# Kernel tuning notes

Hardware: AMD Instinct MI355X
Metric: run time of the kernel (lower is better)

## Reference

```python
import jax, jax.numpy as jnp
import numpy as np

EPS = 1e-5
D, C, T, H = 512, 256, 2, 2  # d_model, d_ctx, tokens, heads
HD = D // H                   # head dim


def _ln(x, g, b):
    m = x.mean(-1, keepdims=True)
    v = ((x - m) ** 2).mean(-1, keepdims=True)
    return (x - m) / jnp.sqrt(v + EPS) * g + b


def setup_inputs() -> dict:
    key = jax.random.key(0)
    ks = jax.random.split(key, 16)
    B, L = 8, 4096
    w = lambda k, s: (jax.random.normal(k, s, jnp.float32) * 0.02)
    Hc, H2 = 512, 1024  # ctx-head hidden = max(D,C); mix hidden = 2*D
    return {
        "x": jax.random.normal(ks[0], (B, L, D), jnp.float32),
        "context": jax.random.normal(ks[1], (B, C), jnp.float32),
        "pad_valid_mask": jax.random.bernoulli(ks[2], 0.9, (B, L)),
        "film_ln_g": jnp.ones(D), "film_ln_b": jnp.zeros(D),
        "film_w": w(ks[3], (2 * D, C)), "film_b": jnp.zeros(2 * D),
        "concat_w": w(ks[4], (D, D + C)), "concat_b": jnp.zeros(D),
        "concat_ln_g": jnp.ones(D), "concat_ln_b": jnp.zeros(D),
        "ctx_w1": w(ks[5], (Hc, C)), "ctx_b1": jnp.zeros(Hc),
        "ctx_w2": w(ks[6], (T * D, Hc)), "ctx_b2": jnp.zeros(T * D),
        "q_ln_g": jnp.ones(D), "q_ln_b": jnp.zeros(D),
        "in_proj_w": w(ks[7], (3 * D, D)), "in_proj_b": jnp.zeros(3 * D),
        "out_proj_w": w(ks[8], (D, D)), "out_proj_b": jnp.zeros(D),
        "mix_w1": w(ks[9], (H2, 4 * D)), "mix_b1": jnp.zeros(H2),
        "mix_w2": w(ks[10], (D, H2)), "mix_b2": jnp.zeros(D),
        "out_ln_g": jnp.ones(D), "out_ln_b": jnp.zeros(D),
        "gate_w": w(ks[11], (D, C)), "gate_b": jnp.zeros(D),
    }


def reference(x, context, pad_valid_mask,
              film_ln_g, film_ln_b, film_w, film_b,
              concat_w, concat_b, concat_ln_g, concat_ln_b,
              ctx_w1, ctx_b1, ctx_w2, ctx_b2,
              q_ln_g, q_ln_b, in_proj_w, in_proj_b, out_proj_w, out_proj_b,
              mix_w1, mix_b1, mix_w2, mix_b2,
              out_ln_g, out_ln_b, gate_w, gate_b):
    B, L, _ = x.shape
    film_gain, alpha_max = 1.0, 1.0
    # 1) HyperFiLM: base = (1 + gain*gamma) * LN(x) + gain*beta
    gb = context @ film_w.T + film_b                      # [B, 2D]
    gamma, beta = gb[:, :D], gb[:, D:]
    base = (1.0 + film_gain * gamma)[:, None, :] * _ln(x, film_ln_g, film_ln_b) \
           + (film_gain * beta)[:, None, :]
    # 2) Concat path
    ctx_exp = jnp.broadcast_to(context[:, None, :], (B, L, C))
    z = jnp.concatenate([x, ctx_exp], axis=-1)            # [B, L, D+C]
    upd_c = _ln(jax.nn.relu(z @ concat_w.T + concat_b), concat_ln_g, concat_ln_b)
    # 3) Cross-attn path: context -> T tokens
    h = jax.nn.gelu(context @ ctx_w1.T + ctx_b1, approximate=False)
    ctx_tok = (h @ ctx_w2.T + ctx_b2).reshape(B, T, D)
    x_q = _ln(x, q_ln_g, q_ln_b)
    wq, wk, wv = in_proj_w[:D], in_proj_w[D:2 * D], in_proj_w[2 * D:]
    bq, bk, bv = in_proj_b[:D], in_proj_b[D:2 * D], in_proj_b[2 * D:]
    q = (x_q @ wq.T + bq).reshape(B, L, H, HD)
    k = (ctx_tok @ wk.T + bk).reshape(B, T, H, HD)
    v = (ctx_tok @ wv.T + bv).reshape(B, T, H, HD)
    scores = jnp.einsum('blhd,bthd->bhlt', q, k) / jnp.sqrt(jnp.float32(HD))
    attn = jax.nn.softmax(scores, axis=-1)
    a = jnp.einsum('bhlt,bthd->blhd', attn, v).reshape(B, L, D)
    attn_out = a @ out_proj_w.T + out_proj_b
    mix_in = jnp.concatenate([x, attn_out, x - attn_out, x * attn_out], axis=-1)
    upd_a = jax.nn.relu(mix_in @ mix_w1.T + mix_b1) @ mix_w2.T + mix_b2
    # 4) Combine with sigmoid gate, alpha, pad mask
    gate = jax.nn.sigmoid(context @ gate_w.T + gate_b) * alpha_max  # [B, D]
    gate = gate[:, None, :] * pad_valid_mask[:, :, None].astype(x.dtype)
    out = _ln(base + gate * (upd_c + upd_a), out_ln_g, out_ln_b)
    return out
```

## Files before the change

kernel.cpp:

```cpp
#include <hip/hip_runtime.h>
#include <hip/hip_bf16.h>


#define N_TOK 32768
#define HALF_ROWS 16384

typedef unsigned short u16;
typedef __attribute__((ext_vector_type(8))) __bf16 bf16x8;
typedef __attribute__((ext_vector_type(4))) float f32x4;

__device__ __forceinline__ float bf2f(unsigned int h) { return __uint_as_float(h << 16); }
__device__ __forceinline__ u16 f2bf(float f) {
    unsigned int u = __float_as_uint(f);
    u += 0x7FFFu + ((u >> 16) & 1u);
    return (u16)(u >> 16);
}
__device__ __forceinline__ void load8(const u16* p, float* v) {
    uint4 u = *(const uint4*)p;
    v[0] = bf2f(u.x & 0xffffu); v[1] = bf2f(u.x >> 16);
    v[2] = bf2f(u.y & 0xffffu); v[3] = bf2f(u.y >> 16);
    v[4] = bf2f(u.z & 0xffffu); v[5] = bf2f(u.z >> 16);
    v[6] = bf2f(u.w & 0xffffu); v[7] = bf2f(u.w >> 16);
}
__device__ __forceinline__ uint4 pack8(const float* v) {
    uint4 u;
    u.x = (unsigned)f2bf(v[0]) | ((unsigned)f2bf(v[1]) << 16);
    u.y = (unsigned)f2bf(v[2]) | ((unsigned)f2bf(v[3]) << 16);
    u.z = (unsigned)f2bf(v[4]) | ((unsigned)f2bf(v[5]) << 16);
    u.w = (unsigned)f2bf(v[6]) | ((unsigned)f2bf(v[7]) << 16);
    return u;
}
__device__ __forceinline__ void async16(const u16* g, u16* lds) {
    __builtin_amdgcn_global_load_lds(
        (const __attribute__((address_space(1))) unsigned int*)g,
        (__attribute__((address_space(3))) unsigned int*)lds, 16, 0, 0);
}

__global__ void prep_kernel(const float* __restrict__ in_proj_w,
                            const float* __restrict__ in_proj_b,
                            const float* __restrict__ qb,
                            const float* __restrict__ concat_w,
                            const float* __restrict__ mix_w1,
                            const float* __restrict__ mix_w2,
                            const float* __restrict__ context,
                            float* __restrict__ bqp,
                            u16* __restrict__ cwbf, u16* __restrict__ m1bf,
                            u16* __restrict__ m2bf, u16* __restrict__ ctxbf) {
    const int bid = blockIdx.x;
    const int tid = threadIdx.x;
    if (bid < 128) {
        const int wave = tid >> 6, lane = tid & 63;
        const int j = bid * 4 + wave;
        const int i = lane * 8;
        float4 w0 = *(const float4*)(in_proj_w + (size_t)j * 512 + i);
        float4 w1 = *(const float4*)(in_proj_w + (size_t)j * 512 + i + 4);
        float4 b0 = *(const float4*)(qb + i);
        float4 b1 = *(const float4*)(qb + i + 4);
        float p1 = w0.x*b0.x + w0.y*b0.y + w0.z*b0.z + w0.w*b0.w
                 + w1.x*b1.x + w1.y*b1.y + w1.z*b1.z + w1.w*b1.w;
        for (int m = 1; m < 64; m <<= 1) p1 += __shfl_xor(p1, m, 64);
        if (lane == 0) bqp[j] = in_proj_b[j] + p1;
    } else if (bid < 320) {
        int i = (bid - 128) * 256 + tid;
        const float* s = concat_w + (size_t)i * 8;
        float4 a = *(const float4*)s;
        float4 b = *(const float4*)(s + 4);
        float v[8] = {a.x, a.y, a.z, a.w, b.x, b.y, b.z, b.w};
        *(uint4*)(cwbf + (size_t)i * 8) = pack8(v);
    } else if (bid < 576) {
        int i = (bid - 320) * 256 + tid;
        const float* s = mix_w2 + (size_t)i * 8;
        float4 a = *(const float4*)s;
        float4 b = *(const float4*)(s + 4);
        float v[8] = {a.x, a.y, a.z, a.w, b.x, b.y, b.z, b.w};
        *(uint4*)(m2bf + (size_t)i * 8) = pack8(v);
    } else if (bid < 1344) {
        int idx = (bid - 576) * 256 + tid;
        int n = idx / 192;
        int k = (idx - n * 192) * 8;
        const float* base = mix_w1 + (size_t)n * 2048;
        float v[8];
        if (k < 512) {
            #pragma unroll
            for (int e = 0; e < 8; e++) v[e] = base[k + e] + base[1024 + k + e];
        } else if (k < 1024) {
            #pragma unroll
            for (int e = 0; e < 8; e++) v[e] = base[k + e] - base[512 + k + e];
        } else {
            #pragma unroll
            for (int e = 0; e < 8; e++) v[e] = base[512 + k + e];
        }
        *(uint4*)(m1bf + (size_t)n * 1536 + k) = pack8(v);
    } else {
        for (int i = tid; i < 2048; i += 256)
            ctxbf[i] = f2bf(context[i]);
    }
}

__global__ void ctx_stage_a(const float* __restrict__ context,
                            const float* __restrict__ film_w, const float* __restrict__ film_b,
                            const float* __restrict__ gate_w, const float* __restrict__ gate_b,
                            const float* __restrict__ ctx_w1, const float* __restrict__ ctx_b1,
                            float* __restrict__ gb1, float* __restrict__ betab,
                            float* __restrict__ gateb, float* __restrict__ hbuf) {
    const int wave = threadIdx.x >> 6, lane = threadIdx.x & 63;
    const int widx = blockIdx.x * 4 + wave;
    const int b   = widx >> 11;
    const int j2  = widx & 2047;
    const int cat = j2 >> 9;
    const int j   = j2 & 511;
    const float* wrow;
    if      (cat == 0) wrow = film_w + (size_t)j * 256;
    else if (cat == 1) wrow = film_w + (size_t)(512 + j) * 256;
    else if (cat == 2) wrow = gate_w + (size_t)j * 256;
    else               wrow = ctx_w1 + (size_t)j * 256;
    float4 wv = *(const float4*)(wrow + lane * 4);
    float4 cv = *(const float4*)(context + b * 256 + lane * 4);
    float s = wv.x * cv.x + wv.y * cv.y + wv.z * cv.z + wv.w * cv.w;
    for (int m = 1; m < 64; m <<= 1) s += __shfl_xor(s, m, 64);
    if (lane == 0) {
        if      (cat == 0) gb1[b * 512 + j]   = 1.0f + s + film_b[j];
        else if (cat == 1) betab[b * 512 + j] = s + film_b[512 + j];
        else if (cat == 2) gateb[b * 512 + j] = 1.f / (1.f + expf(-(s + gate_b[j])));
        else {
            float hv = s + ctx_b1[j];
            hbuf[b * 512 + j] = 0.5f * hv * (1.0f + erff(hv * 0.70710678118654752f));
        }
    }
}

__global__ void ctx_stage_b(const float* __restrict__ hbuf,
                            const float* __restrict__ ctx_w2, const float* __restrict__ ctx_b2,
                            float* __restrict__ tokbuf) {
    const int wave = threadIdx.x >> 6, lane = threadIdx.x & 63;
    const int widx = blockIdx.x * 4 + wave;
    const int b = widx >> 10;
    const int j = widx & 1023;
    const float* wrow = ctx_w2 + (size_t)j * 512 + lane * 8;
    const float* hr   = hbuf + b * 512 + lane * 8;
    float4 w0 = *(const float4*)wrow, w1 = *(const float4*)(wrow + 4);
    float4 h0 = *(const float4*)hr,   h1 = *(const float4*)(hr + 4);
    float s = w0.x*h0.x + w0.y*h0.y + w0.z*h0.z + w0.w*h0.w
            + w1.x*h1.x + w1.y*h1.y + w1.z*h1.z + w1.w*h1.w;
    for (int m = 1; m < 64; m <<= 1) s += __shfl_xor(s, m, 64);
    if (lane == 0) tokbuf[b * 1024 + j] = s + ctx_b2[j];
}

__global__ void ctx_stage_c(const float* __restrict__ tokbuf,
                            const float* __restrict__ in_proj_w, const float* __restrict__ in_proj_b,
                            float* __restrict__ kbuf, float* __restrict__ vbuf) {
    const int wave = threadIdx.x >> 6, lane = threadIdx.x & 63;
    const int widx = blockIdx.x * 4 + wave;
    const int b  = widx >> 11;
    const int r  = widx & 2047;
    const int t  = r >> 10;
    const int kv = (r >> 9) & 1;
    const int j  = r & 511;
    const float* wrow = in_proj_w + (size_t)(512 + kv * 512 + j) * 512 + lane * 8;
    const float* tk   = tokbuf + (b * 2 + t) * 512 + lane * 8;
    float4 w0 = *(const float4*)wrow, w1 = *(const float4*)(wrow + 4);
    float4 t0 = *(const float4*)tk,   t1 = *(const float4*)(tk + 4);
    float s = w0.x*t0.x + w0.y*t0.y + w0.z*t0.z + w0.w*t0.w
            + w1.x*t1.x + w1.y*t1.y + w1.z*t1.z + w1.w*t1.w;
    for (int m = 1; m < 64; m <<= 1) s += __shfl_xor(s, m, 64);
    if (lane == 0) {
        float v = s + in_proj_b[512 + kv * 512 + j];
        if (kv == 0) kbuf[(b * 2 + t) * 512 + j] = v;
        else         vbuf[(b * 2 + t) * 512 + j] = v;
    }
}

__global__ void ctx_stage_d(const float* __restrict__ in_proj_w,
                            const float* __restrict__ out_proj_w,
                            const float* __restrict__ qg, const float* __restrict__ bqp,
                            const float* __restrict__ kbuf, const float* __restrict__ vbuf,
                            float* __restrict__ ubuf, float* __restrict__ vobuf,
                            float* __restrict__ subuf, float* __restrict__ c0buf) {
    const int tid = threadIdx.x;
    __shared__ float sh[256];
    __shared__ float red[256];
    if (blockIdx.x < 32) {
        const int bid = blockIdx.x;
        const int b = bid >> 2, idx = bid & 3;
        const int t = idx >> 1, h = idx & 1;
        sh[tid] = kbuf[(b * 2 + t) * 512 + h * 256 + tid];
        __syncthreads();
        float a0 = 0.f, a1 = 0.f;
        #pragma unroll 4
        for (int dd = 0; dd < 256; dd++) {
            const float kv = sh[dd];
            const float* wr = in_proj_w + (size_t)(h * 256 + dd) * 512;
            a0 += kv * wr[tid];
            a1 += kv * wr[tid + 256];
        }
        float u0 = a0 * qg[tid], u1 = a1 * qg[tid + 256];
        ubuf[bid * 512 + tid]       = u0;
        ubuf[bid * 512 + tid + 256] = u1;
        red[tid] = u0 + u1;
        __syncthreads();
        for (int s = 128; s > 0; s >>= 1) { if (tid < s) red[tid] += red[tid + s]; __syncthreads(); }
        if (tid == 0) subuf[bid] = red[0];
        __syncthreads();
        red[tid] = bqp[h * 256 + tid] * sh[tid];
        __syncthreads();
        for (int s = 128; s > 0; s >>= 1) { if (tid < s) red[tid] += red[tid + s]; __syncthreads(); }
        if (tid == 0) c0buf[bid] = red[0];
    } else {
        const int bid = blockIdx.x - 32;
        const int b = bid >> 2, idx = bid & 3;
        const int t = idx >> 1, h = idx & 1;
        sh[tid] = vbuf[(b * 2 + t) * 512 + h * 256 + tid];
        __syncthreads();
        const float* w0 = out_proj_w + (size_t)tid * 512 + h * 256;
        const float* w1 = out_proj_w + (size_t)(tid + 256) * 512 + h * 256;
        float acc0 = 0.f, acc1 = 0.f;
        #pragma unroll 2
        for (int dd = 0; dd < 256; dd += 4) {
            float4 x0 = *(const float4*)(w0 + dd);
            float4 x1 = *(const float4*)(w1 + dd);
            acc0 += x0.x*sh[dd] + x0.y*sh[dd+1] + x0.z*sh[dd+2] + x0.w*sh[dd+3];
            acc1 += x1.x*sh[dd] + x1.y*sh[dd+1] + x1.z*sh[dd+2] + x1.w*sh[dd+3];
        }
        vobuf[bid * 512 + tid]       = acc0;
        vobuf[bid * 512 + tid + 256] = acc1;
    }
}

__global__ void statsattn_kernel(const float* __restrict__ x, float* __restrict__ stats,
                                 u16* __restrict__ mixA, u16* __restrict__ pbufH,
                                 const float* __restrict__ ubuf, const float* __restrict__ subuf,
                                 const float* __restrict__ c0buf, const float* __restrict__ vobuf,
                                 const float* __restrict__ ob, const int rowbase) {
    const int wave = threadIdx.x >> 6, lane = threadIdx.x & 63;
    const size_t lr = (size_t)blockIdx.x * 8 + wave * 2;
    const size_t gr = lr + rowbase;
    const int b = (int)(gr >> 12);
    float v[2][8], s[2] = {0.f, 0.f}, ss[2] = {0.f, 0.f};
    #pragma unroll
    for (int r = 0; r < 2; r++) {
        const float* xr = x + (gr + r) * 512 + lane * 8;
        float4 a = *(const float4*)xr;
        float4 c = *(const float4*)(xr + 4);
        v[r][0]=a.x; v[r][1]=a.y; v[r][2]=a.z; v[r][3]=a.w;
        v[r][4]=c.x; v[r][5]=c.y; v[r][6]=c.z; v[r][7]=c.w;
        #pragma unroll
        for (int e = 0; e < 8; e++) { s[r] += v[r][e]; ss[r] += v[r][e] * v[r][e]; }
    }
    float u[4][8];
    #pragma unroll
    for (int idx = 0; idx < 4; idx++) {
        const float* up = ubuf + (b * 4 + idx) * 512 + lane * 8;
        float4 u0 = *(const float4*)up, u1 = *(const float4*)(up + 4);
        u[idx][0]=u0.x; u[idx][1]=u0.y; u[idx][2]=u0.z; u[idx][3]=u0.w;
        u[idx][4]=u1.x; u[idx][5]=u1.y; u[idx][6]=u1.z; u[idx][7]=u1.w;
    }
    float sd[2][4];
    #pragma unroll
    for (int r = 0; r < 2; r++)
        #pragma unroll
        for (int idx = 0; idx < 4; idx++) {
            float acc = 0.f;
            #pragma unroll
            for (int e = 0; e < 8; e++) acc += v[r][e] * u[idx][e];
            sd[r][idx] = acc;
        }
    for (int m = 1; m < 64; m <<= 1) {
        #pragma unroll
        for (int r = 0; r < 2; r++) {
            s[r] += __shfl_xor(s[r], m, 64); ss[r] += __shfl_xor(ss[r], m, 64);
            #pragma unroll
            for (int idx = 0; idx < 4; idx++) sd[r][idx] += __shfl_xor(sd[r][idx], m, 64);
        }
    }
    float vo[4][8];
    #pragma unroll
    for (int idx = 0; idx < 4; idx++) {
        const float* vp = vobuf + (b * 4 + idx) * 512 + lane * 8;
        float4 v0 = *(const float4*)vp, v1 = *(const float4*)(vp + 4);
        vo[idx][0]=v0.x; vo[idx][1]=v0.y; vo[idx][2]=v0.z; vo[idx][3]=v0.w;
        vo[idx][4]=v1.x; vo[idx][5]=v1.y; vo[idx][6]=v1.z; vo[idx][7]=v1.w;
    }
    float obp[8];
    {
        const float* op = ob + lane * 8;
        float4 o0 = *(const float4*)op, o1 = *(const float4*)(op + 4);
        obp[0]=o0.x; obp[1]=o0.y; obp[2]=o0.z; obp[3]=o0.w;
        obp[4]=o1.x; obp[5]=o1.y; obp[6]=o1.z; obp[7]=o1.w;
    }
    #pragma unroll
    for (int r = 0; r < 2; r++) {
        const float mean = s[r] * (1.f / 512.f);
        const float rstd = rsqrtf(ss[r] * (1.f / 512.f) - mean * mean + 1e-5f);
        if (lane == 0) { stats[(gr + r) * 2] = mean; stats[(gr + r) * 2 + 1] = rstd; }
        float sc[4];
        #pragma unroll
        for (int idx = 0; idx < 4; idx++)
            sc[idx] = (rstd * (sd[r][idx] - mean * subuf[b * 4 + idx]) + c0buf[b * 4 + idx]) * (1.f / 16.f);
        float p[4];
        #pragma unroll
        for (int h = 0; h < 2; h++) {
            float s0 = sc[h], s1 = sc[2 + h];
            float mx = fmaxf(s0, s1);
            float e0 = expf(s0 - mx), e1 = expf(s1 - mx);
            float inv = 1.f / (e0 + e1);
            p[h] = e0 * inv; p[2 + h] = e1 * inv;
        }
        float o[8], pr[8];
        #pragma unroll
        for (int e = 0; e < 8; e++) {
            o[e] = p[0]*vo[0][e] + p[1]*vo[1][e] + p[2]*vo[2][e] + p[3]*vo[3][e] + obp[e];
            pr[e] = v[r][e] * o[e];
        }
        *(uint4*)(mixA + (gr + r) * 1024 + lane * 8)       = pack8(v[r]);
        *(uint4*)(mixA + (gr + r) * 1024 + 512 + lane * 8) = pack8(o);
        *(uint4*)(pbufH + (lr + r) * 512 + lane * 8)       = pack8(pr);
    }
}

template<int AMODE, bool RELU>
__launch_bounds__(256)
__global__ void mfma_gemm(const u16* __restrict__ A0, const u16* __restrict__ A1,
                          const u16* __restrict__ Wb, const float* __restrict__ bias,
                          u16* __restrict__ out, const int K, const int lda, const int ldo) {
    __shared__ __align__(16) u16 S[16384];
    u16* As = S;
    u16* Bs = S + 8192;
    const int tid = threadIdx.x;
    const int w = tid >> 6, l = tid & 63;
    const int wm = w >> 1, wn = w & 1;
    const size_t m0 = (size_t)blockIdx.x * 128;
    const int n0 = blockIdx.y * 128;
    const int rb = w * 8 + (l >> 3);
    const int kswz = ((l & 7) ^ (l >> 3)) * 8;
    const int bidx = (int)(m0 >> 12);
    const int quad = l >> 4, lc = l & 15;

    f32x4 acc[4][4];
    #pragma unroll
    for (int i = 0; i < 4; i++)
        #pragma unroll
        for (int j = 0; j < 4; j++) acc[i][j] = (f32x4){0.f, 0.f, 0.f, 0.f};

    for (int k0 = 0; k0 < K; k0 += 64) {
        __syncthreads();
        if constexpr (AMODE == 0) {
            #pragma unroll
            for (int r = 0; r < 4; r++)
                async16(A0 + (m0 + r * 32 + rb) * (size_t)lda + k0 + kswz, &As[r * 2048 + w * 512]);
        } else if constexpr (AMODE == 1) {
            if (k0 < 512) {
                #pragma unroll
                for (int r = 0; r < 4; r++)
                    async16(A0 + (m0 + r * 32 + rb) * (size_t)lda + k0 + kswz, &As[r * 2048 + w * 512]);
            } else {
                #pragma unroll
                for (int r = 0; r < 4; r++)
                    async16(A1 + bidx * 256 + (k0 - 512) + kswz, &As[r * 2048 + w * 512]);
            }
        } else {
            if (k0 < 1024) {
                #pragma unroll
                for (int r = 0; r < 4; r++)
                    async16(A0 + (m0 + r * 32 + rb) * (size_t)1024 + k0 + kswz, &As[r * 2048 + w * 512]);
            } else {
                #pragma unroll
                for (int r = 0; r < 4; r++)
                    async16(A1 + (m0 + r * 32 + rb) * (size_t)512 + (k0 - 1024) + kswz, &As[r * 2048 + w * 512]);
            }
        }
        #pragma unroll
        for (int r = 0; r < 4; r++)
            async16(Wb + (size_t)(n0 + r * 32 + rb) * K + k0 + kswz, &Bs[r * 2048 + w * 512]);
        __syncthreads();
        #pragma unroll
        for (int kk = 0; kk < 2; kk++) {
            bf16x8 af[4], bff[4];
            #pragma unroll
            for (int t = 0; t < 4; t++) {
                const int ch = ((kk << 2) | quad) ^ (lc & 7);
                af[t]  = *(const bf16x8*)&As[(wm * 64 + t * 16 + lc) * 64 + ch * 8];
                bff[t] = *(const bf16x8*)&Bs[(wn * 64 + t * 16 + lc) * 64 + ch * 8];
            }
            #pragma unroll
            for (int i = 0; i < 4; i++)
                #pragma unroll
                for (int j = 0; j < 4; j++)
                    acc[i][j] = __builtin_amdgcn_mfma_f32_16x16x32_bf16(af[i], bff[j], acc[i][j], 0, 0, 0);
        }
    }

    float bv[4];
    #pragma unroll
    for (int j = 0; j < 4; j++) bv[j] = bias[n0 + wn * 64 + j * 16 + lc];
    const int erow = tid >> 2;
    const int ecb  = (tid & 3) * 32;
    __syncthreads();
    #pragma unroll
    for (int p = 0; p < 2; p++) {
        if (p) __syncthreads();
        if (wm == p) {
            #pragma unroll
            for (int i = 0; i < 4; i++)
                #pragma unroll
                for (int j = 0; j < 4; j++)
                    #pragma unroll
                    for (int reg = 0; reg < 4; reg++) {
                        float vv = acc[i][j][reg] + bv[j];
                        if (RELU) vv = fmaxf(vv, 0.f);
                        S[(i * 16 + quad * 4 + reg) * 136 + wn * 64 + j * 16 + lc] = f2bf(vv);
                    }
        }
        __syncthreads();
        #pragma unroll
        for (int q = 0; q < 4; q++)
            *(uint4*)(out + (m0 + p * 64 + erow) * (size_t)ldo + n0 + ecb + q * 8)
                = *(const uint4*)&S[erow * 136 + ecb + q * 8];
    }
}

__global__ void final_kernel(const u16* __restrict__ mixA, const float* __restrict__ stats,
                             const u16* __restrict__ bufc,
                             const float* __restrict__ cg, const float* __restrict__ cb,
                             const float* __restrict__ gb1, const float* __restrict__ betab,
                             const float* __restrict__ gateb, const int* __restrict__ mask,
                             const float* __restrict__ fg, const float* __restrict__ fb,
                             const float* __restrict__ og, const float* __restrict__ ob,
                             float* __restrict__ out) {
    const int wave = threadIdx.x >> 6, lane = threadIdx.x & 63;
    const size_t row = (size_t)blockIdx.x * 4 + wave;
    const int b = (int)(row >> 12);
    const int c0 = lane * 8;
    float xv[8], uc[8], ua[8];
    load8(mixA + row * 1024 + c0, xv);
    load8(mixA + row * 1024 + 512 + c0, ua);
    load8(bufc + row * 512 + c0, uc);
    float sc = 0.f, ssc = 0.f;
    #pragma unroll
    for (int e = 0; e < 8; e++) { sc += uc[e]; ssc += uc[e] * uc[e]; }
    for (int m = 1; m < 64; m <<= 1) { sc += __shfl_xor(sc, m, 64); ssc += __shfl_xor(ssc, m, 64); }
    const float mc = sc * (1.f / 512.f);
    const float rc = rsqrtf(ssc * (1.f / 512.f) - mc * mc + 1e-5f);
    const float mean = stats[row * 2], rstd = stats[row * 2 + 1];
    const float mf = (mask[row] != 0) ? 1.f : 0.f;
    float y[8];
    float s = 0.f, ss = 0.f;
    #pragma unroll
    for (int e = 0; e < 8; e++) {
        int c = c0 + e;
        float ucn = (uc[e] - mc) * rc * cg[c] + cb[c];
        float xh = (xv[e] - mean) * rstd;
        float base = gb1[b * 512 + c] * (xh * fg[c] + fb[c]) + betab[b * 512 + c];
        float yv = base + gateb[b * 512 + c] * mf * (ucn + ua[e]);
        y[e] = yv; s += yv; ss += yv * yv;
    }
    for (int m = 1; m < 64; m <<= 1) { s += __shfl_xor(s, m, 64); ss += __shfl_xor(ss, m, 64); }
    float mean2 = s * (1.f / 512.f);
    float rstd2 = rsqrtf(ss * (1.f / 512.f) - mean2 * mean2 + 1e-5f);
    float o[8];
    #pragma unroll
    for (int e = 0; e < 8; e++) {
        int c = c0 + e;
        o[e] = (y[e] - mean2) * rstd2 * og[c] + ob[c];
    }
    *(float4*)(out + row * 512 + c0)     = make_float4(o[0], o[1], o[2], o[3]);
    *(float4*)(out + row * 512 + c0 + 4) = make_float4(o[4], o[5], o[6], o[7]);
}

extern "C" void kernel_launch(void* const* d_in, const int* in_sizes, int n_in,
                              void* d_out, int out_size, void* d_ws, size_t ws_size,
                              hipStream_t stream) {
    const float* x          = (const float*)d_in[0];
    const float* context    = (const float*)d_in[1];
    const int*   mask       = (const int*)d_in[2];
    const float* film_ln_g  = (const float*)d_in[3];
    const float* film_ln_b  = (const float*)d_in[4];
    const float* film_w     = (const float*)d_in[5];
    const float* film_b     = (const float*)d_in[6];
    const float* concat_w   = (const float*)d_in[7];
    const float* concat_b   = (const float*)d_in[8];
    const float* concat_ln_g= (const float*)d_in[9];
    const float* concat_ln_b= (const float*)d_in[10];
    const float* ctx_w1     = (const float*)d_in[11];
    const float* ctx_b1     = (const float*)d_in[12];
    const float* ctx_w2     = (const float*)d_in[13];
    const float* ctx_b2     = (const float*)d_in[14];
    const float* q_ln_g     = (const float*)d_in[15];
    const float* q_ln_b     = (const float*)d_in[16];
    const float* in_proj_w  = (const float*)d_in[17];
    const float* in_proj_b  = (const float*)d_in[18];
    const float* out_proj_w = (const float*)d_in[19];
    const float* out_proj_b = (const float*)d_in[20];
    const float* mix_w1     = (const float*)d_in[21];
    const float* mix_b1     = (const float*)d_in[22];
    const float* mix_w2     = (const float*)d_in[23];
    const float* mix_b2     = (const float*)d_in[24];
    const float* out_ln_g   = (const float*)d_in[25];
    const float* out_ln_b   = (const float*)d_in[26];
    const float* gate_w     = (const float*)d_in[27];
    const float* gate_b     = (const float*)d_in[28];
    float* out = (float*)d_out;

    float* gb1    = (float*)d_ws;
    float* betab  = gb1 + 4096;
    float* gateb  = betab + 4096;
    float* kbuf   = gateb + 4096;
    float* vbuf   = kbuf + 8192;
    float* bqp    = vbuf + 8192;
    float* hbuf   = bqp + 512;
    float* tokbuf = hbuf + 4096;
    float* ubuf   = tokbuf + 8192;
    float* vobuf  = ubuf + 16384;
    float* subuf  = vobuf + 16384;
    float* c0buf  = subuf + 32;
    float* stats  = c0buf + 32;
    u16* ctxbf = (u16*)(stats + 65536);
    u16* cwbf  = ctxbf + 2048;
    u16* m1bf  = cwbf + 393216;
    u16* m2bf  = m1bf + 1572864;
    u16* mixA  = m2bf + 524288;
    u16* bufc  = mixA + (size_t)N_TOK * 1024;
    u16* pbufH = bufc + (size_t)N_TOK * 512;
    u16* bufhH = pbufH + (size_t)HALF_ROWS * 512;

    prep_kernel<<<1345, 256, 0, stream>>>(in_proj_w, in_proj_b, q_ln_b,
                                          concat_w, mix_w1, mix_w2, context,
                                          bqp, cwbf, m1bf, m2bf, ctxbf);
    ctx_stage_a<<<4096, 256, 0, stream>>>(context, film_w, film_b, gate_w, gate_b,
                                          ctx_w1, ctx_b1, gb1, betab, gateb, hbuf);
    ctx_stage_b<<<2048, 256, 0, stream>>>(hbuf, ctx_w2, ctx_b2, tokbuf);
    ctx_stage_c<<<4096, 256, 0, stream>>>(tokbuf, in_proj_w, in_proj_b, kbuf, vbuf);
    ctx_stage_d<<<64, 256, 0, stream>>>(in_proj_w, out_proj_w, q_ln_g, bqp,
                                        kbuf, vbuf, ubuf, vobuf, subuf, c0buf);

    for (int h = 0; h < 2; h++) {
        const int rowbase = h * HALF_ROWS;
        statsattn_kernel<<<HALF_ROWS / 8, 256, 0, stream>>>(
            x, stats, mixA, pbufH, ubuf, subuf, c0buf, vobuf, out_proj_b, rowbase);
        mfma_gemm<2, true><<<dim3(128, 8), 256, 0, stream>>>(
            mixA + (size_t)rowbase * 1024, pbufH, m1bf, mix_b1,
            bufhH, 1536, 1024, 1024);
        mfma_gemm<0, false><<<dim3(128, 4), 256, 0, stream>>>(
            bufhH, nullptr, m2bf, mix_b2,
            mixA + (size_t)rowbase * 1024 + 512, 1024, 1024, 1024);
    }

    mfma_gemm<1, true><<<dim3(256, 4), 256, 0, stream>>>(
        mixA, ctxbf, cwbf, concat_b, bufc, 768, 1024, 512);

    final_kernel<<<N_TOK / 4, 256, 0, stream>>>(mixA, stats, bufc,
                                                concat_ln_g, concat_ln_b,
                                                gb1, betab, gateb, mask,
                                                film_ln_g, film_ln_b,
                                                out_ln_g, out_ln_b, out);
    (void)in_sizes; (void)n_in; (void)out_size; (void)ws_size;
}
```

Before: 497.5 us.

## Replace mix1 GEMM with 256x256-tile double-buffered 8-wave pipelined kernel

Adds a dedicated mix1 GEMM kernel that uses 256x256 output tiles with 512 threads and 128 KB of dynamic LDS. Global-to-LDS async loads for the next K tile are double-buffered and interleaved with MFMA quadrants, using explicit vmcnt waits, barriers and setprio. This is meant to raise arithmetic intensity per loaded byte and hide load latency behind MFMA work, which the old 128x128 single-buffered loop exposed. The cost is larger LDS use, lower occupancy, and fragile hand-written wait counts. The now-unused AMODE 2 path is removed from the generic GEMM.

```diff
diff --git a/kernel.cpp b/kernel.cpp
--- a/kernel.cpp
+++ b/kernel.cpp
@@ -35,6 +35,11 @@
         (const __attribute__((address_space(1))) unsigned int*)g,
         (__attribute__((address_space(3))) unsigned int*)lds, 16, 0, 0);
 }
+
+#define FENCE() asm volatile("" ::: "memory")
+#define BARRIER() do { FENCE(); __builtin_amdgcn_s_barrier(); FENCE(); } while (0)
+#define WAITV(n) asm volatile("s_waitcnt vmcnt(" #n ")" ::: "memory")
+#define LGKM0()  asm volatile("s_waitcnt lgkmcnt(0)" ::: "memory")
 
 __global__ void prep_kernel(const float* __restrict__ in_proj_w,
                             const float* __restrict__ in_proj_b,
@@ -347,7 +352,7 @@
             #pragma unroll
             for (int r = 0; r < 4; r++)
                 async16(A0 + (m0 + r * 32 + rb) * (size_t)lda + k0 + kswz, &As[r * 2048 + w * 512]);
-        } else if constexpr (AMODE == 1) {
+        } else {
             if (k0 < 512) {
                 #pragma unroll
                 for (int r = 0; r < 4; r++)
@@ -357,16 +362,6 @@
                 for (int r = 0; r < 4; r++)
                     async16(A1 + bidx * 256 + (k0 - 512) + kswz, &As[r * 2048 + w * 512]);
             }
-        } else {
-            if (k0 < 1024) {
-                #pragma unroll
-                for (int r = 0; r < 4; r++)
-                    async16(A0 + (m0 + r * 32 + rb) * (size_t)1024 + k0 + kswz, &As[r * 2048 + w * 512]);
-            } else {
-                #pragma unroll
-                for (int r = 0; r < 4; r++)
-                    async16(A1 + (m0 + r * 32 + rb) * (size_t)512 + (k0 - 1024) + kswz, &As[r * 2048 + w * 512]);
-            }
         }
         #pragma unroll
         for (int r = 0; r < 4; r++)
@@ -415,6 +410,150 @@
         for (int q = 0; q < 4; q++)
             *(uint4*)(out + (m0 + p * 64 + erow) * (size_t)ldo + n0 + ecb + q * 8)
                 = *(const uint4*)&S[erow * 136 + ecb + q * 8];
+    }
+}
+
+__launch_bounds__(512, 2)
+__global__ void mix1_gemm8(const u16* __restrict__ A0, const u16* __restrict__ A1,
+                           const u16* __restrict__ Wb, const float* __restrict__ bias,
+                           u16* __restrict__ out) {
+    extern __shared__ __align__(16) u16 S[];
+    u16* As = S;
+    u16* Bs = S + 32768;
+    const int tid = threadIdx.x;
+    const int l = tid & 63;
+    const int w = tid >> 6;
+    const int wm = w >> 2, wn = w & 3;
+    const int quad = l >> 4, lc = l & 15;
+    const size_t m0 = (size_t)blockIdx.x * 256;
+    const int n0 = blockIdx.y * 256;
+
+    const int r0 = tid >> 3;
+    const int r1 = (tid + 512) >> 3;
+    const int c0s = ((tid & 7) ^ (r0 & 7)) * 8;
+    const int c1s = ((tid & 7) ^ (r1 & 7)) * 8;
+
+    auto stA = [&](int kt, int h, int buf) {
+        u16* dst = As + (buf * 2 + h) * 8192;
+        if (kt < 16) {
+            async16(A0 + (m0 + h * 128 + r0) * 1024 + kt * 64 + c0s, dst + tid * 8);
+            async16(A0 + (m0 + h * 128 + r1) * 1024 + kt * 64 + c1s, dst + (tid + 512) * 8);
+        } else {
+            async16(A1 + (m0 + h * 128 + r0) * 512 + (kt - 16) * 64 + c0s, dst + tid * 8);
+            async16(A1 + (m0 + h * 128 + r1) * 512 + (kt - 16) * 64 + c1s, dst + (tid + 512) * 8);
+        }
+    };
+    auto stB = [&](int kt, int h, int buf) {
+        u16* dst = Bs + (buf * 2 + h) * 8192;
+        async16(Wb + (size_t)(n0 + h * 128 + r0) * 1536 + kt * 64 + c0s, dst + tid * 8);
+        async16(Wb + (size_t)(n0 + h * 128 + r1) * 1536 + kt * 64 + c1s, dst + (tid + 512) * 8);
+    };
+
+    bf16x8 a_[4][2], b_[2][2][2];
+    f32x4 acc[8][4];
+    #pragma unroll
+    for (int i = 0; i < 8; i++)
+        #pragma unroll
+        for (int j = 0; j < 4; j++) acc[i][j] = (f32x4){0.f, 0.f, 0.f, 0.f};
+
+    auto rdA = [&](int buf, int qi) {
+        const u16* Ab = As + (buf * 2 + wm) * 8192;
+        #pragma unroll
+        for (int ii = 0; ii < 4; ii++) {
+            const int r = (qi * 4 + ii) * 16 + lc;
+            #pragma unroll
+            for (int kk = 0; kk < 2; kk++) {
+                const int cs = (kk * 4 + quad) ^ (r & 7);
+                a_[ii][kk] = *(const bf16x8*)&Ab[r * 64 + cs * 8];
+            }
+        }
+    };
+    auto rdB = [&](int buf, int qj) {
+        #pragma unroll
+        for (int jj = 0; jj < 2; jj++) {
+            const int nr = wn * 64 + (qj * 2 + jj) * 16 + lc;
+            const int hb = nr >> 7, r = nr & 127;
+            const u16* Bb = Bs + (buf * 2 + hb) * 8192;
+            #pragma unroll
+            for (int kk = 0; kk < 2; kk++) {
+                const int cs = (kk * 4 + quad) ^ (r & 7);
+                b_[qj][jj][kk] = *(const bf16x8*)&Bb[r * 64 + cs * 8];
+            }
+        }
+    };
+    auto mfma16 = [&](int qi, int qj) {
+        __builtin_amdgcn_s_setprio(1);
+        #pragma unroll
+        for (int ii = 0; ii < 4; ii++)
+            #pragma unroll
+            for (int jj = 0; jj < 2; jj++)
+                #pragma unroll
+                for (int kk = 0; kk < 2; kk++)
+                    acc[qi * 4 + ii][qj * 2 + jj] = __builtin_amdgcn_mfma_f32_16x16x32_bf16(
+                        a_[ii][kk], b_[qj][jj][kk], acc[qi * 4 + ii][qj * 2 + jj], 0, 0, 0);
+        __builtin_amdgcn_s_setprio(0);
+    };
+
+    stA(0, 0, 0); stA(0, 1, 0); stB(0, 0, 0); stB(0, 1, 0);
+    stA(1, 0, 1);
+    WAITV(2); BARRIER();
+
+    for (int it = 0; it < 12; it++) {
+        const int tb = 2 * it + 1;
+        const bool more = (it < 11);
+        rdA(0, 0); rdB(0, 0);
+        stA(tb, 1, 1);
+        BARRIER(); mfma16(0, 0);
+        rdB(0, 1);
+        stB(tb, 0, 1);
+        BARRIER(); mfma16(0, 1);
+        rdA(0, 1);
+        stB(tb, 1, 1);
+        BARRIER(); mfma16(1, 1);
+        BARRIER();
+        if (more) { stA(tb + 1, 0, 0); WAITV(2); }
+        else      { WAITV(0); }
+        BARRIER(); mfma16(1, 0);
+        rdA(1, 0); rdB(1, 0);
+        if (more) stA(tb + 1, 1, 0);
+        BARRIER(); mfma16(0, 0);
+        rdB(1, 1);
+        if (more) stB(tb + 1, 0, 0);
+        BARRIER(); mfma16(0, 1);
+        rdA(1, 1);
+        if (more) stB(tb + 1, 1, 0);
+        BARRIER(); mfma16(1, 1);
+        BARRIER();
+        if (more) { stA(tb + 2, 0, 1); WAITV(2); }
+        BARRIER(); mfma16(1, 0);
+    }
+
+    BARRIER();
+    float bv[4];
+    #pragma unroll
+    for (int j = 0; j < 4; j++) bv[j] = bias[n0 + wn * 64 + j * 16 + lc];
+    #pragma unroll
+    for (int p = 0; p < 2; p++) {
+        if (p) BARRIER();
+        if (wm == p) {
+            #pragma unroll
+            for (int i = 0; i < 8; i++)
+                #pragma unroll
+                for (int j = 0; j < 4; j++)
+                    #pragma unroll
+                    for (int reg = 0; reg < 4; reg++) {
+                        float vv = fmaxf(acc[i][j][reg] + bv[j], 0.f);
+                        S[(i * 16 + quad * 4 + reg) * 264 + wn * 64 + j * 16 + lc] = f2bf(vv);
+                    }
+        }
+        LGKM0(); BARRIER();
+        #pragma unroll
+        for (int kq = 0; kq < 8; kq++) {
+            const int cix = tid + kq * 512;
+            const int row = cix >> 5, ch = cix & 31;
+            *(uint4*)(out + (m0 + p * 128 + row) * 1024 + n0 + ch * 8)
+                = *(const uint4*)&S[row * 264 + ch * 8];
+        }
     }
 }
 
@@ -522,6 +661,13 @@
     u16* pbufH = bufc + (size_t)N_TOK * 512;
     u16* bufhH = pbufH + (size_t)HALF_ROWS * 512;
 
+    static bool attr_set = false;
+    if (!attr_set) {
+        hipFuncSetAttribute((const void*)mix1_gemm8,
+                            hipFuncAttributeMaxDynamicSharedMemorySize, 131072);
+        attr_set = true;
+    }
+
     prep_kernel<<<1345, 256, 0, stream>>>(in_proj_w, in_proj_b, q_ln_b,
                                           concat_w, mix_w1, mix_w2, context,
                                           bqp, cwbf, m1bf, m2bf, ctxbf);
@@ -536,9 +682,8 @@
         const int rowbase = h * HALF_ROWS;
         statsattn_kernel<<<HALF_ROWS / 8, 256, 0, stream>>>(
             x, stats, mixA, pbufH, ubuf, subuf, c0buf, vobuf, out_proj_b, rowbase);
-        mfma_gemm<2, true><<<dim3(128, 8), 256, 0, stream>>>(
-            mixA + (size_t)rowbase * 1024, pbufH, m1bf, mix_b1,
-            bufhH, 1536, 1024, 1024);
+        mix1_gemm8<<<dim3(64, 4), 512, 131072, stream>>>(
+            mixA + (size_t)rowbase * 1024, pbufH, m1bf, mix_b1, bufhH);
         mfma_gemm<0, false><<<dim3(128, 4), 256, 0, stream>>>(
             bufhH, nullptr, m2bf, mix_b2,
             mixA + (size_t)rowbase * 1024 + 512, 1024, 1024, 1024);
```

After: 460.6 us. 1.08x faster.
